# Performance work log

Measured on AMD Instinct MI355X. Metric: run time of the kernel, lower is better.

Reference implementation:

```python
import jax, jax.numpy as jnp
import numpy as np

EMBED_DIM = 1024
NUM_HEADS = 16
HEAD_DIM = EMBED_DIM // NUM_HEADS
SEG_LENS = [1024, 2048, 4096]
DIL_RATIOS = [1, 2, 4]
NEG = -1e8  # lse fill value used by sparse_to_dense


def setup_inputs() -> dict:
    root = jax.random.key(0)
    ks = jax.random.split(root, 12)
    B, L, E = 1, 4096, EMBED_DIM
    s = 0.02
    return {
        "query": jax.random.normal(ks[0], (B, L, E), jnp.float32),
        "key": jax.random.normal(ks[1], (B, L, E), jnp.float32),
        "value": jax.random.normal(ks[2], (B, L, E), jnp.float32),
        "Wq": jax.random.normal(ks[3], (E, E), jnp.float32) * s,
        "bq": jnp.zeros((E,), jnp.float32),
        "Wk": jax.random.normal(ks[4], (E, E), jnp.float32) * s,
        "bk": jnp.zeros((E,), jnp.float32),
        "Wv": jax.random.normal(ks[5], (E, E), jnp.float32) * s,
        "bv": jnp.zeros((E,), jnp.float32),
        "Wo": jax.random.normal(ks[6], (E, E), jnp.float32) * s,
        "bo": jnp.zeros((E,), jnp.float32),
    }


def _branch(q, k, v, sl, dr, L):
    """One (segment_length, dilated_ratio) branch.
    q,k,v: (B, L, H, D). Returns dense out (B, H, L, D) and lse (B, H, L).
    """
    B = q.shape[0]
    H, D = NUM_HEADS, HEAD_DIM
    sl = min(sl, L)
    pad = (-L) % sl
    if pad:
        pw = ((0, 0), (0, pad), (0, 0), (0, 0))
        q, k, v = jnp.pad(q, pw), jnp.pad(k, pw), jnp.pad(v, pw)
    n = (L + pad) // sl  # segments
    qs = q.reshape(B * n, sl, H, D)
    ks = k.reshape(B * n, sl, H, D)
    vs = v.reshape(B * n, sl, H, D)
    # dense_to_sparse: head j (group r = j // (H//dr)) keeps positions i*dr + r
    hg = H // dr
    g = sl // dr
    grp = jnp.arange(H) // hg                      # (H,)
    pos = jnp.arange(g)[:, None] * dr + grp[None]  # (g, H) dense positions
    hidx = jnp.arange(H)[None, :]
    sp = lambda x: x[:, pos, hidx, :]              # (B*n, g, H, D)
    qd, kd, vd = sp(qs), sp(ks), sp(vs)
    # causal attention within each sparse segment (flash_attn semantics)
    scores = jnp.einsum('bqhd,bkhd->bhqk', qd, kd) * (D ** -0.5)
    mask = jnp.tril(jnp.ones((g, g), bool))
    scores = jnp.where(mask, scores, -jnp.inf)
    lse = jax.nn.logsumexp(scores, axis=-1)        # (B*n, H, g)
    o = jnp.einsum('bhqk,bkhd->bqhd', jnp.exp(scores - lse[..., None]), vd)
    # sparse_to_dense: scatter back onto dense positions, NEG elsewhere
    hcol = jnp.arange(H)[:, None]                  # (H,1)
    od = jnp.zeros((B * n, H, sl, D), o.dtype).at[:, hcol, pos.T].set(
        o.transpose(0, 2, 1, 3))
    ld = jnp.zeros((B * n, H, sl), lse.dtype).at[:, hcol, pos.T].set(lse)
    ld = jnp.where(ld == 0.0, NEG, ld)  # matches masked_fill_(lse == 0, -1e8)
    od = od.reshape(B, n, H, sl, D).transpose(0, 2, 1, 3, 4)
    od = od.reshape(B, H, n * sl, D)[:, :, :L]
    ld = ld.reshape(B, n, H, sl).transpose(0, 2, 1, 3).reshape(B, H, n * sl)[:, :, :L]
    return od, ld


def reference(query, key, value, Wq, bq, Wk, bk, Wv, bv, Wo, bo):
    B, L, E = query.shape
    H, D = NUM_HEADS, HEAD_DIM
    q = (query @ Wq.T + bq).reshape(B, L, H, D)
    k = (key @ Wk.T + bk).reshape(B, L, H, D)
    v = (value @ Wv.T + bv).reshape(B, L, H, D)
    outs, lses = [], []
    for sl, dr in zip(SEG_LENS, DIL_RATIOS):
        o, l = _branch(q, k, v, sl, dr, L)
        outs.append(o)
        lses.append(l)
    lse_all = jnp.stack(lses, 0)[..., None]        # (nb, B, H, L, 1)
    m = lse_all.max(0)
    w = jnp.exp(lse_all - m)
    w = w / w.sum(0)                               # softmax merge weights
    w = jax.lax.stop_gradient(w)                   # torch computes under no_grad
    out = sum(o * wi.astype(o.dtype) for o, wi in zip(outs, w))  # (B,H,L,D)
    out = out.transpose(0, 2, 1, 3).reshape(B, L, E)
    return out @ Wo.T + bo
```

## Files before the change

kernel.cpp:

```cpp
#include <hip/hip_runtime.h>
#include <math.h>


#define L_SEQ 4096
#define EDIM  1024
#define NH    16
#define HD    64
#define GLEN  1024

typedef __bf16 bf16;
typedef __bf16 bf16x8 __attribute__((ext_vector_type(8)));
typedef __bf16 bf16x4 __attribute__((ext_vector_type(4)));
typedef short  s16x4  __attribute__((ext_vector_type(4)));
typedef float  f32x4  __attribute__((ext_vector_type(4)));

__device__ __forceinline__ void gload16(const bf16* g, bf16* l) {
  __builtin_amdgcn_global_load_lds(
      (__attribute__((address_space(1))) void*)(const_cast<bf16*>(g)),
      (__attribute__((address_space(3))) void*)(l),
      16, 0, 0);
}

__device__ __forceinline__ f32x4 mfma16x16x16_bf16(bf16x4 a, bf16x4 b, f32x4 c) {
#if defined(__HIP_DEVICE_COMPILE__)
  union { bf16x4 h; s16x4 s; } ua, ub;
  ua.h = a; ub.h = b;
  return __builtin_amdgcn_mfma_f32_16x16x16bf16_1k(ua.s, ub.s, c, 0, 0, 0);
#else
  (void)a; (void)b;
  return c;
#endif
}

__global__ __launch_bounds__(256) void cvt_kernel(
    const float* q, const float* k, const float* v,
    const float* wq, const float* wk, const float* wv, const float* wo,
    bf16* oq, bf16* ok, bf16* ov,
    bf16* owq, bf16* owk, bf16* owv, bf16* owo)
{
  const float* src; bf16* dst; int n;
  switch (blockIdx.y) {
    case 0: src = q;  dst = oq;  n = L_SEQ*EDIM; break;
    case 1: src = k;  dst = ok;  n = L_SEQ*EDIM; break;
    case 2: src = v;  dst = ov;  n = L_SEQ*EDIM; break;
    case 3: src = wq; dst = owq; n = EDIM*EDIM; break;
    case 4: src = wk; dst = owk; n = EDIM*EDIM; break;
    case 5: src = wv; dst = owv; n = EDIM*EDIM; break;
    default: src = wo; dst = owo; n = EDIM*EDIM; break;
  }
  int i = (blockIdx.x * 256 + threadIdx.x) * 8;
  if (i >= n) return;
  const float4* s4 = (const float4*)(src + i);
  float4 a = s4[0], b = s4[1];
  bf16x8 o = { (bf16)a.x, (bf16)a.y, (bf16)a.z, (bf16)a.w,
               (bf16)b.x, (bf16)b.y, (bf16)b.z, (bf16)b.w };
  *(bf16x8*)(dst + i) = o;
}

template <typename OutT>
__device__ __forceinline__ void gemm_body(const bf16* __restrict__ A,
                                          const bf16* __restrict__ W,
                                          const float* __restrict__ bias,
                                          OutT* __restrict__ C)
{
  constexpr int K = 1024;
  __shared__ __align__(16) bf16 lA[128 * 32];
  __shared__ __align__(16) bf16 lB[128 * 32];

  const int tid  = threadIdx.x;
  const int lane = tid & 63;
  const int w    = tid >> 6;
  const int quad = lane >> 4;
  const int l16  = lane & 15;
  const int wr   = w >> 1, wc = w & 1;
  const int row0 = blockIdx.y * 128;
  const int col0 = blockIdx.x * 128;

  f32x4 acc[4][4] = {};

  const int c0 = tid, c1 = tid + 256;
  const bf16* Ab0 = A + (size_t)(row0 + (c0 >> 2)) * K + (c0 & 3) * 8;
  const bf16* Ab1 = A + (size_t)(row0 + (c1 >> 2)) * K + (c1 & 3) * 8;
  const bf16* Bb0 = W + (size_t)(col0 + (c0 >> 2)) * K + (c0 & 3) * 8;
  const bf16* Bb1 = W + (size_t)(col0 + (c1 >> 2)) * K + (c1 & 3) * 8;
  bf16* lA0 = &lA[c0 * 8]; bf16* lA1 = &lA[c1 * 8];
  bf16* lB0 = &lB[c0 * 8]; bf16* lB1 = &lB[c1 * 8];

  for (int kt = 0; kt < K; kt += 32) {
    __syncthreads();
    gload16(Ab0 + kt, lA0);
    gload16(Ab1 + kt, lA1);
    gload16(Bb0 + kt, lB0);
    gload16(Bb1 + kt, lB1);
    __syncthreads();

    bf16x8 af[4], bfrag[4];
#pragma unroll
    for (int mi = 0; mi < 4; mi++)
      af[mi] = *(const bf16x8*)&lA[(wr * 64 + mi * 16 + l16) * 32 + quad * 8];
#pragma unroll
    for (int ni = 0; ni < 4; ni++)
      bfrag[ni] = *(const bf16x8*)&lB[(wc * 64 + ni * 16 + l16) * 32 + quad * 8];
#pragma unroll
    for (int mi = 0; mi < 4; mi++)
#pragma unroll
      for (int ni = 0; ni < 4; ni++)
        acc[mi][ni] = __builtin_amdgcn_mfma_f32_16x16x32_bf16(
            af[mi], bfrag[ni], acc[mi][ni], 0, 0, 0);
  }

#pragma unroll
  for (int mi = 0; mi < 4; mi++) {
#pragma unroll
    for (int ni = 0; ni < 4; ni++) {
      const int gcol = col0 + wc * 64 + ni * 16 + l16;
      const float bv = bias[gcol];
#pragma unroll
      for (int r = 0; r < 4; r++) {
        const int grow = row0 + wr * 64 + mi * 16 + quad * 4 + r;
        C[(size_t)grow * 1024 + gcol] = (OutT)(acc[mi][ni][r] + bv);
      }
    }
  }
}

__global__ __launch_bounds__(256) void gemm_qkv_kernel(
    const bf16* xq, const bf16* xk, const bf16* xv,
    const bf16* wq, const bf16* wk, const bf16* wv,
    const float* bq, const float* bk, const float* bv,
    bf16* q, bf16* k, bf16* v)
{
  const bf16 *A, *W; const float* bias; bf16* C;
  if (blockIdx.z == 0)      { A = xq; W = wq; bias = bq; C = q; }
  else if (blockIdx.z == 1) { A = xk; W = wk; bias = bk; C = k; }
  else                      { A = xv; W = wv; bias = bv; C = v; }
  gemm_body<bf16>(A, W, bias, C);
}

__global__ __launch_bounds__(256) void gemm_out_kernel(
    const bf16* A, const bf16* W, const float* bias, float* C)
{
  gemm_body<float>(A, W, bias, C);
}

__global__ __launch_bounds__(256) void vtrans_kernel(
    const bf16* __restrict__ v, bf16* vt0, bf16* vt1, bf16* vt2)
{
  __shared__ __align__(16) bf16 ltile[64 * 72];
  const int bid = blockIdx.x;
  int sl, dr, rem, shift; bf16* vt;
  if (bid < 1024)      { sl = 1024; dr = 1; rem = bid;        vt = vt0; shift = 4; }
  else if (bid < 1536) { sl = 2048; dr = 2; rem = bid - 1024; vt = vt1; shift = 3; }
  else                 { sl = 4096; dr = 4; rem = bid - 1536; vt = vt2; shift = 2; }
  const int ktile = rem & 15;
  const int h     = (rem >> 4) & 15;
  const int seg   = rem >> 8;
  const int grp   = h >> shift;
  const int segbase = seg * sl;
  const int tid = threadIdx.x;
  {
    const int i = tid >> 2, dc = tid & 3;
    const size_t p = (size_t)(segbase + (ktile * 64 + i) * dr + grp);
    const bf16* src = v + p * EDIM + h * 64 + dc * 16;
    *(uint4*)&ltile[i * 72 + dc * 16]     = *(const uint4*)(src);
    *(uint4*)&ltile[i * 72 + dc * 16 + 8] = *(const uint4*)(src + 8);
  }
  __syncthreads();
  {
    const int d = tid >> 2, kc = tid & 3;
    __align__(16) bf16 tmp[16];
#pragma unroll
    for (int j = 0; j < 16; j++) tmp[j] = ltile[(kc * 16 + j) * 72 + d];
    bf16* dst = vt + ((size_t)(seg * NH + h) * 64 + d) * GLEN + ktile * 64 + kc * 16;
    *(uint4*)dst       = *(uint4*)&tmp[0];
    *(uint4*)(dst + 8) = *(uint4*)&tmp[8];
  }
}

__global__ __launch_bounds__(256) void attn_kernel(
    const bf16* __restrict__ qg, const bf16* __restrict__ kg,
    const bf16* vt0, const bf16* vt1, const bf16* vt2,
    bf16* o0, bf16* o1, bf16* o2,
    float* l0, float* l1, float* l2)
{
  __shared__ __align__(16) bf16 lK[2][64 * 64];
  __shared__ __align__(16) bf16 lV[2][64 * 64];

  const int bid = blockIdx.x;
  int sl, dr, rem, shift;
  const bf16* vt; bf16* ob; float* lseb;
  if (bid < 1024)      { sl = 1024; dr = 1; rem = bid;        vt = vt0; ob = o0; lseb = l0; shift = 4; }
  else if (bid < 1536) { sl = 2048; dr = 2; rem = bid - 1024; vt = vt1; ob = o1; lseb = l1; shift = 3; }
  else                 { sl = 4096; dr = 4; rem = bid - 1536; vt = vt2; ob = o2; lseb = l2; shift = 2; }
  const int qt  = 15 - (rem & 15);
  const int h   = (rem >> 4) & 15;
  const int seg = rem >> 8;
  const int grp = h >> shift;
  const int segbase = seg * sl;

  const int tid = threadIdx.x, lane = tid & 63, w = tid >> 6;
  const int quad = lane >> 4, l16 = lane & 15;
  const int qs0 = qt * 64;

  bf16x8 qa0, qa1;
  {
    const int qi = qs0 + w * 16 + l16;
    const size_t p = (size_t)(segbase + qi * dr + grp);
    const bf16* qp = qg + p * EDIM + h * 64 + quad * 8;
    qa0 = *(const bf16x8*)(qp);
    qa1 = *(const bf16x8*)(qp + 32);
  }

  f32x4 Oa[4] = {};
  float m_r = -__builtin_inff(), l_r = 0.f;

  const bf16* vbase = vt + (size_t)(seg * NH + h) * 64 * GLEN;
  const int c0 = tid, c1 = tid + 256;
  const int r0 = c0 >> 3, sw0 = ((c0 & 7) ^ (r0 & 7));
  const int r1 = c1 >> 3, sw1 = ((c1 & 7) ^ (r1 & 7));

  auto stage = [&](int kt, int buf) {
    const bf16* kp0 = kg + (size_t)(segbase + (kt * 64 + r0) * dr + grp) * EDIM + h * 64 + sw0 * 8;
    const bf16* kp1 = kg + (size_t)(segbase + (kt * 64 + r1) * dr + grp) * EDIM + h * 64 + sw1 * 8;
    gload16(kp0, &lK[buf][c0 * 8]);
    gload16(kp1, &lK[buf][c1 * 8]);
    const bf16* vp0 = vbase + (size_t)r0 * GLEN + kt * 64 + sw0 * 8;
    const bf16* vp1 = vbase + (size_t)r1 * GLEN + kt * 64 + sw1 * 8;
    gload16(vp0, &lV[buf][c0 * 8]);
    gload16(vp1, &lV[buf][c1 * 8]);
  };

  stage(0, 0);

  const int qi_lane = qs0 + w * 16 + l16;

  for (int kt = 0; kt <= qt; kt++) {
    __syncthreads();
    if (kt < qt) stage(kt + 1, (kt + 1) & 1);
    const bf16* bK = lK[kt & 1];
    const bf16* bV = lV[kt & 1];

    const bool diag = (kt == qt);
    const int tmax = diag ? w : 3;

    f32x4 s[4];
#pragma unroll
    for (int t = 0; t < 4; t++) {
      if (t <= tmax) {
        s[t] = f32x4{0.f, 0.f, 0.f, 0.f};
        const int kj = t * 16 + l16;
        const int rs = kj & 7;
        bf16x8 ka0 = *(const bf16x8*)&bK[kj * 64 + ((quad       ^ rs) * 8)];
        bf16x8 ka1 = *(const bf16x8*)&bK[kj * 64 + (((4 + quad) ^ rs) * 8)];
        s[t] = __builtin_amdgcn_mfma_f32_16x16x32_bf16(ka0, qa0, s[t], 0, 0, 0);
        s[t] = __builtin_amdgcn_mfma_f32_16x16x32_bf16(ka1, qa1, s[t], 0, 0, 0);
      }
    }

    float p[4][4];
    float mloc = -__builtin_inff();
#pragma unroll
    for (int t = 0; t < 4; t++) {
      if (t <= tmax) {
#pragma unroll
        for (int r = 0; r < 4; r++) {
          float sv = s[t][r] * 0.125f;
          if (diag) {
            const int kj = kt * 64 + t * 16 + quad * 4 + r;
            if (kj > qi_lane) sv = -__builtin_inff();
          }
          p[t][r] = sv;
          mloc = fmaxf(mloc, sv);
        }
      }
    }
    mloc = fmaxf(mloc, __shfl_xor(mloc, 16, 64));
    mloc = fmaxf(mloc, __shfl_xor(mloc, 32, 64));
    const float mnew  = fmaxf(m_r, mloc);
    const float alpha = __expf(m_r - mnew);
    m_r = mnew;

    bf16x4 pb[4];
    float rs_sum = 0.f;
#pragma unroll
    for (int t = 0; t < 4; t++) {
      if (t <= tmax) {
#pragma unroll
        for (int r = 0; r < 4; r++) {
          const float pv = __expf(p[t][r] - mnew);
          pb[t][r] = (bf16)pv;
          rs_sum += pv;
        }
      }
    }
    rs_sum += __shfl_xor(rs_sum, 16, 64);
    rs_sum += __shfl_xor(rs_sum, 32, 64);
    l_r = l_r * alpha + rs_sum;

#pragma unroll
    for (int nf = 0; nf < 4; nf++) {
#pragma unroll
      for (int r = 0; r < 4; r++) Oa[nf][r] *= alpha;
    }

#pragma unroll
    for (int t = 0; t < 4; t++) {
      if (t <= tmax) {
        const int ck  = 2 * t + (quad >> 1);
        const int sub = (quad & 1) * 4;
#pragma unroll
        for (int nf = 0; nf < 4; nf++) {
          const int drow = nf * 16 + l16;
          bf16x4 va = *(const bf16x4*)&bV[drow * 64 + ((ck ^ (drow & 7)) * 8) + sub];
          Oa[nf] = mfma16x16x16_bf16(va, pb[t], Oa[nf]);
        }
      }
    }
  }

  const float linv = 1.0f / l_r;
  const int pdense = segbase + qi_lane * dr + grp;
  bf16* orow = ob + (size_t)pdense * EDIM + h * 64;
#pragma unroll
  for (int nf = 0; nf < 4; nf++) {
    bf16x4 ov;
#pragma unroll
    for (int r = 0; r < 4; r++) ov[r] = (bf16)(Oa[nf][r] * linv);
    *(bf16x4*)(orow + nf * 16 + quad * 4) = ov;
  }
  if (quad == 0)
    lseb[h * L_SEQ + pdense] = m_r + __logf(l_r);
}

__global__ __launch_bounds__(256) void merge_kernel(
    const bf16* __restrict__ o0, const bf16* __restrict__ o1, const bf16* __restrict__ o2,
    const float* __restrict__ l0, const float* __restrict__ l1, const float* __restrict__ l2,
    bf16* __restrict__ merged)
{
  const int idx = blockIdx.x * 256 + threadIdx.x;
  const int dc = idx & 7;
  const int h  = (idx >> 3) & 15;
  const int p  = idx >> 7;
  const bool c1 = ((p & 1) == (h >> 3));
  const bool c2 = ((p & 3) == (h >> 2));
  const float s0 = l0[h * L_SEQ + p];
  const float s1 = c1 ? l1[h * L_SEQ + p] : -__builtin_inff();
  const float s2 = c2 ? l2[h * L_SEQ + p] : -__builtin_inff();
  const float mx = fmaxf(s0, fmaxf(s1, s2));
  float w0 = __expf(s0 - mx);
  float w1 = c1 ? __expf(s1 - mx) : 0.f;
  float w2 = c2 ? __expf(s2 - mx) : 0.f;
  const float inv = 1.0f / (w0 + w1 + w2);
  w0 *= inv; w1 *= inv; w2 *= inv;

  const size_t off = (size_t)p * EDIM + h * 64 + dc * 8;
  float acc[8];
  bf16x8 a0 = *(const bf16x8*)(o0 + off);
#pragma unroll
  for (int j = 0; j < 8; j++) acc[j] = w0 * (float)a0[j];
  if (c1) {
    bf16x8 a1 = *(const bf16x8*)(o1 + off);
#pragma unroll
    for (int j = 0; j < 8; j++) acc[j] += w1 * (float)a1[j];
  }
  if (c2) {
    bf16x8 a2 = *(const bf16x8*)(o2 + off);
#pragma unroll
    for (int j = 0; j < 8; j++) acc[j] += w2 * (float)a2[j];
  }
  bf16x8 r;
#pragma unroll
  for (int j = 0; j < 8; j++) r[j] = (bf16)acc[j];
  *(bf16x8*)(merged + off) = r;
}

extern "C" void kernel_launch(void* const* d_in, const int* in_sizes, int n_in,
                              void* d_out, int out_size, void* d_ws, size_t ws_size,
                              hipStream_t stream)
{
  (void)in_sizes; (void)n_in; (void)out_size; (void)ws_size;
  const float* query = (const float*)d_in[0];
  const float* key   = (const float*)d_in[1];
  const float* value = (const float*)d_in[2];
  const float* Wq = (const float*)d_in[3];
  const float* bq = (const float*)d_in[4];
  const float* Wk = (const float*)d_in[5];
  const float* bk = (const float*)d_in[6];
  const float* Wv = (const float*)d_in[7];
  const float* bv = (const float*)d_in[8];
  const float* Wo = (const float*)d_in[9];
  const float* bo = (const float*)d_in[10];

  char* base = (char*)d_ws;
  size_t off = 0;
  auto take = [&](size_t nbytes) -> char* {
    char* p = base + off;
    off += (nbytes + 255) & ~(size_t)255;
    return p;
  };
  const size_t LE2 = (size_t)L_SEQ * EDIM * 2;
  const size_t EE2 = (size_t)EDIM * EDIM * 2;
  bf16* xq  = (bf16*)take(LE2);
  bf16* xk  = (bf16*)take(LE2);
  bf16* xv  = (bf16*)take(LE2);
  bf16* wqb = (bf16*)take(EE2);
  bf16* wkb = (bf16*)take(EE2);
  bf16* wvb = (bf16*)take(EE2);
  bf16* wob = (bf16*)take(EE2);
  bf16* qb  = (bf16*)take(LE2);
  bf16* kb  = (bf16*)take(LE2);
  bf16* vb  = (bf16*)take(LE2);
  bf16* vt0 = (bf16*)take((size_t)4 * NH * HD * GLEN * 2);
  bf16* vt1 = (bf16*)take((size_t)2 * NH * HD * GLEN * 2);
  bf16* vt2 = (bf16*)take((size_t)1 * NH * HD * GLEN * 2);
  float* lse0 = (float*)take((size_t)NH * L_SEQ * 4);
  float* lse1 = (float*)take((size_t)NH * L_SEQ * 4);
  float* lse2 = (float*)take((size_t)NH * L_SEQ * 4);
  bf16* merged = (bf16*)take(LE2);
  bf16* o0 = xq; bf16* o1 = xk; bf16* o2 = xv;

  dim3 blk(256);
  cvt_kernel<<<dim3(2048, 7), blk, 0, stream>>>(
      query, key, value, Wq, Wk, Wv, Wo, xq, xk, xv, wqb, wkb, wvb, wob);
  gemm_qkv_kernel<<<dim3(8, 32, 3), blk, 0, stream>>>(
      xq, xk, xv, wqb, wkb, wvb, bq, bk, bv, qb, kb, vb);
  vtrans_kernel<<<dim3(1792), blk, 0, stream>>>(vb, vt0, vt1, vt2);
  attn_kernel<<<dim3(1792), blk, 0, stream>>>(
      qb, kb, vt0, vt1, vt2, o0, o1, o2, lse0, lse1, lse2);
  merge_kernel<<<dim3(2048), blk, 0, stream>>>(
      o0, o1, o2, lse0, lse1, lse2, merged);
  gemm_out_kernel<<<dim3(8, 32), blk, 0, stream>>>(merged, wob, bo, (float*)d_out);
}
```

Baseline: 258.3 us.

## Process 128-query tiles per attention block with 8 waves sharing K/V tiles

Each attention block now covers two 64-row query tiles, using 512 threads in two wave groups that share the staged K/V tiles in LDS. The grid is halved, and each thread issues one async load per K and V tile instead of two. This is meant to cut redundant global K/V traffic and staging work per query. In exchange, the wave group handling the lower query tile idles on the final K/V tile because of the causal mask, blocks are larger, and fewer blocks are available to balance load.

```diff
diff --git a/kernel.cpp b/kernel.cpp
--- a/kernel.cpp
+++ b/kernel.cpp
@@ -177,7 +177,7 @@
   }
 }
 
-__global__ __launch_bounds__(256) void attn_kernel(
+__global__ __launch_bounds__(512) void attn_kernel(
     const bf16* __restrict__ qg, const bf16* __restrict__ kg,
     const bf16* vt0, const bf16* vt1, const bf16* vt2,
     bf16* o0, bf16* o1, bf16* o2,
@@ -189,23 +189,26 @@
   const int bid = blockIdx.x;
   int sl, dr, rem, shift;
   const bf16* vt; bf16* ob; float* lseb;
-  if (bid < 1024)      { sl = 1024; dr = 1; rem = bid;        vt = vt0; ob = o0; lseb = l0; shift = 4; }
-  else if (bid < 1536) { sl = 2048; dr = 2; rem = bid - 1024; vt = vt1; ob = o1; lseb = l1; shift = 3; }
-  else                 { sl = 4096; dr = 4; rem = bid - 1536; vt = vt2; ob = o2; lseb = l2; shift = 2; }
-  const int qt  = 15 - (rem & 15);
-  const int h   = (rem >> 4) & 15;
-  const int seg = rem >> 8;
+  if (bid < 512)       { sl = 1024; dr = 1; rem = bid;       vt = vt0; ob = o0; lseb = l0; shift = 4; }
+  else if (bid < 768)  { sl = 2048; dr = 2; rem = bid - 512; vt = vt1; ob = o1; lseb = l1; shift = 3; }
+  else                 { sl = 4096; dr = 4; rem = bid - 768; vt = vt2; ob = o2; lseb = l2; shift = 2; }
+  const int qt2 = 7 - (rem & 7);
+  const int h   = (rem >> 3) & 15;
+  const int seg = rem >> 7;
   const int grp = h >> shift;
   const int segbase = seg * sl;
 
   const int tid = threadIdx.x, lane = tid & 63, w = tid >> 6;
+  const int wg = w >> 2, wl = w & 3;
   const int quad = lane >> 4, l16 = lane & 15;
-  const int qs0 = qt * 64;
+
+  const int kt_d   = 2 * qt2 + wg;
+  const int kt_max = 2 * qt2 + 1;
+  const int qi_lane = qt2 * 128 + wg * 64 + wl * 16 + l16;
 
   bf16x8 qa0, qa1;
   {
-    const int qi = qs0 + w * 16 + l16;
-    const size_t p = (size_t)(segbase + qi * dr + grp);
+    const size_t p = (size_t)(segbase + qi_lane * dr + grp);
     const bf16* qp = qg + p * EDIM + h * 64 + quad * 8;
     qa0 = *(const bf16x8*)(qp);
     qa1 = *(const bf16x8*)(qp + 32);
@@ -215,33 +218,26 @@
   float m_r = -__builtin_inff(), l_r = 0.f;
 
   const bf16* vbase = vt + (size_t)(seg * NH + h) * 64 * GLEN;
-  const int c0 = tid, c1 = tid + 256;
-  const int r0 = c0 >> 3, sw0 = ((c0 & 7) ^ (r0 & 7));
-  const int r1 = c1 >> 3, sw1 = ((c1 & 7) ^ (r1 & 7));
+  const int r0 = tid >> 3, sw0 = ((tid & 7) ^ (r0 & 7));
 
   auto stage = [&](int kt, int buf) {
-    const bf16* kp0 = kg + (size_t)(segbase + (kt * 64 + r0) * dr + grp) * EDIM + h * 64 + sw0 * 8;
-    const bf16* kp1 = kg + (size_t)(segbase + (kt * 64 + r1) * dr + grp) * EDIM + h * 64 + sw1 * 8;
-    gload16(kp0, &lK[buf][c0 * 8]);
-    gload16(kp1, &lK[buf][c1 * 8]);
-    const bf16* vp0 = vbase + (size_t)r0 * GLEN + kt * 64 + sw0 * 8;
-    const bf16* vp1 = vbase + (size_t)r1 * GLEN + kt * 64 + sw1 * 8;
-    gload16(vp0, &lV[buf][c0 * 8]);
-    gload16(vp1, &lV[buf][c1 * 8]);
+    const bf16* kp = kg + (size_t)(segbase + (kt * 64 + r0) * dr + grp) * EDIM + h * 64 + sw0 * 8;
+    gload16(kp, &lK[buf][tid * 8]);
+    const bf16* vp = vbase + (size_t)r0 * GLEN + kt * 64 + sw0 * 8;
+    gload16(vp, &lV[buf][tid * 8]);
   };
 
   stage(0, 0);
 
-  const int qi_lane = qs0 + w * 16 + l16;
-
-  for (int kt = 0; kt <= qt; kt++) {
+  for (int kt = 0; kt <= kt_max; kt++) {
     __syncthreads();
-    if (kt < qt) stage(kt + 1, (kt + 1) & 1);
+    if (kt < kt_max) stage(kt + 1, (kt + 1) & 1);
+    if (kt > kt_d) continue;
     const bf16* bK = lK[kt & 1];
     const bf16* bV = lV[kt & 1];
 
-    const bool diag = (kt == qt);
-    const int tmax = diag ? w : 3;
+    const bool diag = (kt == kt_d);
+    const int tmax = diag ? wl : 3;
 
     f32x4 s[4];
 #pragma unroll
@@ -425,7 +421,7 @@
   gemm_qkv_kernel<<<dim3(8, 32, 3), blk, 0, stream>>>(
       xq, xk, xv, wqb, wkb, wvb, bq, bk, bv, qb, kb, vb);
   vtrans_kernel<<<dim3(1792), blk, 0, stream>>>(vb, vt0, vt1, vt2);
-  attn_kernel<<<dim3(1792), blk, 0, stream>>>(
+  attn_kernel<<<dim3(896), dim3(512), 0, stream>>>(
       qb, kb, vt0, vt1, vt2, o0, o1, o2, lse0, lse1, lse2);
   merge_kernel<<<dim3(2048), blk, 0, stream>>>(
       o0, o1, o2, lse0, lse1, lse2, merged);
```

Result: slower. 271.5 us (+5.1%).

## Pre-pack K into contiguous tiles and stage K/V through registers

Applied to the files above, without the earlier changes.

The V transpose kernel becomes a reshape kernel that also packs the dilated, strided K rows into contiguous 64x64 tiles per segment and head, and V tiles become tile-contiguous too. The attention kernel then loads each K/V tile with coalesced 16-byte global reads into registers, prefetches the next tile into registers, and writes it to a single LDS buffer, replacing the double-buffered async global-to-LDS loads. This removes strided gathers from the attention inner loop and halves LDS use. The cost is an extra pass writing and reading a packed copy of K, plus a second barrier per iteration.

```diff
diff --git a/kernel.cpp b/kernel.cpp
--- a/kernel.cpp
+++ b/kernel.cpp
@@ -143,21 +143,34 @@
   gemm_body<float>(A, W, bias, C);
 }
 
-__global__ __launch_bounds__(256) void vtrans_kernel(
-    const bf16* __restrict__ v, bf16* vt0, bf16* vt1, bf16* vt2)
+__global__ __launch_bounds__(256) void reshape_kernel(
+    const bf16* __restrict__ k, const bf16* __restrict__ v,
+    bf16* kt0, bf16* kt1, bf16* kt2,
+    bf16* vt0, bf16* vt1, bf16* vt2)
 {
   __shared__ __align__(16) bf16 ltile[64 * 72];
   const int bid = blockIdx.x;
-  int sl, dr, rem, shift; bf16* vt;
-  if (bid < 1024)      { sl = 1024; dr = 1; rem = bid;        vt = vt0; shift = 4; }
-  else if (bid < 1536) { sl = 2048; dr = 2; rem = bid - 1024; vt = vt1; shift = 3; }
-  else                 { sl = 4096; dr = 4; rem = bid - 1536; vt = vt2; shift = 2; }
+  int sl, dr, rem, shift; bf16 *ktb, *vtb;
+  if (bid < 1024)      { sl = 1024; dr = 1; rem = bid;        ktb = kt0; vtb = vt0; shift = 4; }
+  else if (bid < 1536) { sl = 2048; dr = 2; rem = bid - 1024; ktb = kt1; vtb = vt1; shift = 3; }
+  else                 { sl = 4096; dr = 4; rem = bid - 1536; ktb = kt2; vtb = vt2; shift = 2; }
   const int ktile = rem & 15;
   const int h     = (rem >> 4) & 15;
   const int seg   = rem >> 8;
   const int grp   = h >> shift;
   const int segbase = seg * sl;
   const int tid = threadIdx.x;
+  const size_t tOff = ((size_t)((seg * NH + h) * 16 + ktile)) * 4096;
+
+  {
+#pragma unroll
+    for (int half = 0; half < 2; half++) {
+      const int p   = tid + half * 256;
+      const int kjl = p >> 3, dc = p & 7;
+      const bf16* src = k + (size_t)(segbase + (ktile * 64 + kjl) * dr + grp) * EDIM + h * 64 + dc * 8;
+      *(uint4*)(ktb + tOff + p * 8) = *(const uint4*)src;
+    }
+  }
   {
     const int i = tid >> 2, dc = tid & 3;
     const size_t p = (size_t)(segbase + (ktile * 64 + i) * dr + grp);
@@ -171,27 +184,28 @@
     __align__(16) bf16 tmp[16];
 #pragma unroll
     for (int j = 0; j < 16; j++) tmp[j] = ltile[(kc * 16 + j) * 72 + d];
-    bf16* dst = vt + ((size_t)(seg * NH + h) * 64 + d) * GLEN + ktile * 64 + kc * 16;
+    bf16* dst = vtb + tOff + d * 64 + kc * 16;
     *(uint4*)dst       = *(uint4*)&tmp[0];
     *(uint4*)(dst + 8) = *(uint4*)&tmp[8];
   }
 }
 
 __global__ __launch_bounds__(256) void attn_kernel(
-    const bf16* __restrict__ qg, const bf16* __restrict__ kg,
+    const bf16* __restrict__ qg,
+    const bf16* kt0, const bf16* kt1, const bf16* kt2,
     const bf16* vt0, const bf16* vt1, const bf16* vt2,
     bf16* o0, bf16* o1, bf16* o2,
     float* l0, float* l1, float* l2)
 {
-  __shared__ __align__(16) bf16 lK[2][64 * 64];
-  __shared__ __align__(16) bf16 lV[2][64 * 64];
+  __shared__ __align__(16) bf16 lK[64 * 64];
+  __shared__ __align__(16) bf16 lV[64 * 64];
 
   const int bid = blockIdx.x;
   int sl, dr, rem, shift;
-  const bf16* vt; bf16* ob; float* lseb;
-  if (bid < 1024)      { sl = 1024; dr = 1; rem = bid;        vt = vt0; ob = o0; lseb = l0; shift = 4; }
-  else if (bid < 1536) { sl = 2048; dr = 2; rem = bid - 1024; vt = vt1; ob = o1; lseb = l1; shift = 3; }
-  else                 { sl = 4096; dr = 4; rem = bid - 1536; vt = vt2; ob = o2; lseb = l2; shift = 2; }
+  const bf16 *ktb, *vtb; bf16* ob; float* lseb;
+  if (bid < 1024)      { sl = 1024; dr = 1; rem = bid;        ktb = kt0; vtb = vt0; ob = o0; lseb = l0; shift = 4; }
+  else if (bid < 1536) { sl = 2048; dr = 2; rem = bid - 1024; ktb = kt1; vtb = vt1; ob = o1; lseb = l1; shift = 3; }
+  else                 { sl = 4096; dr = 4; rem = bid - 1536; ktb = kt2; vtb = vt2; ob = o2; lseb = l2; shift = 2; }
   const int qt  = 15 - (rem & 15);
   const int h   = (rem >> 4) & 15;
   const int seg = rem >> 8;
@@ -201,11 +215,11 @@
   const int tid = threadIdx.x, lane = tid & 63, w = tid >> 6;
   const int quad = lane >> 4, l16 = lane & 15;
   const int qs0 = qt * 64;
+  const int qi_lane = qs0 + w * 16 + l16;
 
   bf16x8 qa0, qa1;
   {
-    const int qi = qs0 + w * 16 + l16;
-    const size_t p = (size_t)(segbase + qi * dr + grp);
+    const size_t p = (size_t)(segbase + qi_lane * dr + grp);
     const bf16* qp = qg + p * EDIM + h * 64 + quad * 8;
     qa0 = *(const bf16x8*)(qp);
     qa1 = *(const bf16x8*)(qp + 32);
@@ -214,31 +228,33 @@
   f32x4 Oa[4] = {};
   float m_r = -__builtin_inff(), l_r = 0.f;
 
-  const bf16* vbase = vt + (size_t)(seg * NH + h) * 64 * GLEN;
-  const int c0 = tid, c1 = tid + 256;
-  const int r0 = c0 >> 3, sw0 = ((c0 & 7) ^ (r0 & 7));
-  const int r1 = c1 >> 3, sw1 = ((c1 & 7) ^ (r1 & 7));
-
-  auto stage = [&](int kt, int buf) {
-    const bf16* kp0 = kg + (size_t)(segbase + (kt * 64 + r0) * dr + grp) * EDIM + h * 64 + sw0 * 8;
-    const bf16* kp1 = kg + (size_t)(segbase + (kt * 64 + r1) * dr + grp) * EDIM + h * 64 + sw1 * 8;
-    gload16(kp0, &lK[buf][c0 * 8]);
-    gload16(kp1, &lK[buf][c1 * 8]);
-    const bf16* vp0 = vbase + (size_t)r0 * GLEN + kt * 64 + sw0 * 8;
-    const bf16* vp1 = vbase + (size_t)r1 * GLEN + kt * 64 + sw1 * 8;
-    gload16(vp0, &lV[buf][c0 * 8]);
-    gload16(vp1, &lV[buf][c1 * 8]);
-  };
-
-  stage(0, 0);
-
-  const int qi_lane = qs0 + w * 16 + l16;
+  const bf16* kbase = ktb + ((size_t)((seg * NH + h) * 16)) * 4096;
+  const bf16* vbase = vtb + ((size_t)((seg * NH + h) * 16)) * 4096;
+
+  const int p0 = tid, p1 = tid + 256;
+  const int s0 = (p0 >> 3) * 64 + (((p0 & 7) ^ ((p0 >> 3) & 7)) * 8);
+  const int s1 = (p1 >> 3) * 64 + (((p1 & 7) ^ ((p1 >> 3) & 7)) * 8);
+
+  uint4 rk0 = *(const uint4*)(kbase + p0 * 8);
+  uint4 rk1 = *(const uint4*)(kbase + p1 * 8);
+  uint4 rv0 = *(const uint4*)(vbase + p0 * 8);
+  uint4 rv1 = *(const uint4*)(vbase + p1 * 8);
 
   for (int kt = 0; kt <= qt; kt++) {
     __syncthreads();
-    if (kt < qt) stage(kt + 1, (kt + 1) & 1);
-    const bf16* bK = lK[kt & 1];
-    const bf16* bV = lV[kt & 1];
+    *(uint4*)&lK[s0] = rk0;
+    *(uint4*)&lK[s1] = rk1;
+    *(uint4*)&lV[s0] = rv0;
+    *(uint4*)&lV[s1] = rv1;
+    if (kt < qt) {
+      const bf16* kT = kbase + (size_t)(kt + 1) * 4096;
+      const bf16* vT = vbase + (size_t)(kt + 1) * 4096;
+      rk0 = *(const uint4*)(kT + p0 * 8);
+      rk1 = *(const uint4*)(kT + p1 * 8);
+      rv0 = *(const uint4*)(vT + p0 * 8);
+      rv1 = *(const uint4*)(vT + p1 * 8);
+    }
+    __syncthreads();
 
     const bool diag = (kt == qt);
     const int tmax = diag ? w : 3;
@@ -250,8 +266,8 @@
         s[t] = f32x4{0.f, 0.f, 0.f, 0.f};
         const int kj = t * 16 + l16;
         const int rs = kj & 7;
-        bf16x8 ka0 = *(const bf16x8*)&bK[kj * 64 + ((quad       ^ rs) * 8)];
-        bf16x8 ka1 = *(const bf16x8*)&bK[kj * 64 + (((4 + quad) ^ rs) * 8)];
+        bf16x8 ka0 = *(const bf16x8*)&lK[kj * 64 + ((quad       ^ rs) * 8)];
+        bf16x8 ka1 = *(const bf16x8*)&lK[kj * 64 + (((4 + quad) ^ rs) * 8)];
         s[t] = __builtin_amdgcn_mfma_f32_16x16x32_bf16(ka0, qa0, s[t], 0, 0, 0);
         s[t] = __builtin_amdgcn_mfma_f32_16x16x32_bf16(ka1, qa1, s[t], 0, 0, 0);
       }
@@ -311,7 +327,7 @@
 #pragma unroll
         for (int nf = 0; nf < 4; nf++) {
           const int drow = nf * 16 + l16;
-          bf16x4 va = *(const bf16x4*)&bV[drow * 64 + ((ck ^ (drow & 7)) * 8) + sub];
+          bf16x4 va = *(const bf16x4*)&lV[drow * 64 + ((ck ^ (drow & 7)) * 8) + sub];
           Oa[nf] = mfma16x16x16_bf16(va, pb[t], Oa[nf]);
         }
       }
@@ -410,6 +426,9 @@
   bf16* qb  = (bf16*)take(LE2);
   bf16* kb  = (bf16*)take(LE2);
   bf16* vb  = (bf16*)take(LE2);
+  bf16* kt0 = (bf16*)take((size_t)4 * NH * GLEN * HD * 2);
+  bf16* kt1 = (bf16*)take((size_t)2 * NH * GLEN * HD * 2);
+  bf16* kt2 = (bf16*)take((size_t)1 * NH * GLEN * HD * 2);
   bf16* vt0 = (bf16*)take((size_t)4 * NH * HD * GLEN * 2);
   bf16* vt1 = (bf16*)take((size_t)2 * NH * HD * GLEN * 2);
   bf16* vt2 = (bf16*)take((size_t)1 * NH * HD * GLEN * 2);
@@ -424,9 +443,10 @@
       query, key, value, Wq, Wk, Wv, Wo, xq, xk, xv, wqb, wkb, wvb, wob);
   gemm_qkv_kernel<<<dim3(8, 32, 3), blk, 0, stream>>>(
       xq, xk, xv, wqb, wkb, wvb, bq, bk, bv, qb, kb, vb);
-  vtrans_kernel<<<dim3(1792), blk, 0, stream>>>(vb, vt0, vt1, vt2);
+  reshape_kernel<<<dim3(1792), blk, 0, stream>>>(
+      kb, vb, kt0, kt1, kt2, vt0, vt1, vt2);
   attn_kernel<<<dim3(1792), blk, 0, stream>>>(
-      qb, kb, vt0, vt1, vt2, o0, o1, o2, lse0, lse1, lse2);
+      qb, kt0, kt1, kt2, vt0, vt1, vt2, o0, o1, o2, lse0, lse1, lse2);
   merge_kernel<<<dim3(2048), blk, 0, stream>>>(
       o0, o1, o2, lse0, lse1, lse2, merged);
   gemm_out_kernel<<<dim3(8, 32), blk, 0, stream>>>(merged, wob, bo, (float*)d_out);
```

Measured after the change: 262.0 us. Within noise of the previous version (+1.4%).
